# Kernel optimization log

Measured on AMD Instinct MI355X. Metric: run time of the kernel, lower is better.

Reference implementation:

```python
import jax, jax.numpy as jnp
import numpy as np

NEG_INF = -1e9  # matches masked_fill value in torch code
LRELU_ALPHA = 0.2


def setup_inputs() -> dict:
    key = jax.random.key(0)
    k1, k2, k3, k4 = jax.random.split(key, 4)
    B, N, F_IN, H, DK = 4, 2048, 128, 4, 32
    x = jax.random.normal(k1, (B, N, F_IN), dtype=jnp.float32)
    adj = jax.random.randint(k2, (B, N, N), 0, 2, dtype=jnp.int32)
    # xavier-ish scaled params
    W = jax.random.normal(k3, (H, F_IN, DK), dtype=jnp.float32) * (1.0 / np.sqrt(F_IN))
    a = jax.random.normal(k4, (H, 2 * DK, 1), dtype=jnp.float32) * (1.0 / np.sqrt(2 * DK))
    return {"x": x, "adj": adj, "W": W, "a": a}


def reference(x, adj, W, a):
    B, N, _ = x.shape
    H, _, DK = W.shape
    # h: (B, H, N, DK)
    h = jnp.einsum('bni,hio->bhno', x, W)
    # Split attention vector: e[b,h,i,j] = h_i.a_l + h_j.a_r  (avoids O(N^2 * 2d) concat)
    a_l = a[:, :DK, 0]   # (H, DK)
    a_r = a[:, DK:, 0]   # (H, DK)
    el = jnp.einsum('bhnd,hd->bhn', h, a_l)  # (B, H, N)
    er = jnp.einsum('bhnd,hd->bhn', h, a_r)  # (B, H, N)
    e = el[:, :, :, None] + er[:, :, None, :]          # (B, H, N, N)
    e = jax.nn.leaky_relu(e, negative_slope=LRELU_ALPHA)
    e = jnp.where(adj[:, None, :, :] == 0, NEG_INF, e)
    alpha = jax.nn.softmax(e, axis=-1)                 # dropout is identity (eval)
    h_prime = jnp.einsum('bhij,bhjd->bhid', alpha, h)  # (B, H, N, DK)
    # torch code does h_prime.view(B, N, -1) on contiguous (B,H,N,DK): raw reshape
    out = h_prime.reshape(B, N, H * DK)
    return out
```

## Files before the change

kernel.cpp:

```cpp
#include <hip/hip_runtime.h>
#include <stdint.h>

#define LOG2E 1.4426950408889634f

typedef __bf16 v8bf __attribute__((ext_vector_type(8)));
typedef float v16f __attribute__((ext_vector_type(16)));

static constexpr int B = 4, N = 2048, FIN = 128, H = 4, DK = 32;
static constexpr int IT = N / 32;

__device__ __forceinline__ float exp2_fast(float x) {
#if __has_builtin(__builtin_amdgcn_exp2f)
  return __builtin_amdgcn_exp2f(x);
#else
  float r;
  asm("v_exp_f32 %0, %1" : "=v"(r) : "v"(x));
  return r;
#endif
}

__device__ __forceinline__ unsigned int bf16_rne(float f) {
  unsigned int u = __builtin_bit_cast(unsigned int, f);
  u += 0x7FFFu + ((u >> 16) & 1u);
  return u >> 16;
}

__global__ __launch_bounds__(256) void k_prep(const float* __restrict__ x,
                                              const float* __restrict__ W,
                                              unsigned short* __restrict__ xb,
                                              unsigned short* __restrict__ wtb) {
  int idx = blockIdx.x * 256 + threadIdx.x;
  constexpr int TX = B * N * FIN;
  if (idx < TX) {
    xb[idx] = (unsigned short)bf16_rne(x[idx]);
  } else {
    int j = idx - TX;
    int h = j >> 12, r = j & 4095, d = r >> 7, f = r & 127;
    wtb[j] = (unsigned short)bf16_rne(W[(h * FIN + f) * DK + d]);
  }
}

__global__ __launch_bounds__(256) void k_pack(const int* __restrict__ adj,
                                              unsigned int* __restrict__ adjb) {
  int wid = (blockIdx.x * 256 + threadIdx.x) >> 6;
  int lane = threadIdx.x & 63;
  const int* p = adj + (size_t)wid * 256 + lane;
  unsigned long long m0 = __ballot(p[0] != 0);
  unsigned long long m1 = __ballot(p[64] != 0);
  unsigned long long m2 = __ballot(p[128] != 0);
  unsigned long long m3 = __ballot(p[192] != 0);
  if (lane == 0) {
    uint4 v0 = {(unsigned)m0, (unsigned)(m0 >> 32), (unsigned)m1, (unsigned)(m1 >> 32)};
    uint4 v1 = {(unsigned)m2, (unsigned)(m2 >> 32), (unsigned)m3, (unsigned)(m3 >> 32)};
    uint4* dst = (uint4*)(adjb + (size_t)wid * 8);
    dst[0] = v0;
    dst[1] = v1;
  }
}

__global__ __launch_bounds__(256) void k_hproj(const unsigned short* __restrict__ xb,
                                               const unsigned short* __restrict__ wtb,
                                               const float* __restrict__ a,
                                               unsigned short* __restrict__ h_t,
                                               float* __restrict__ el,
                                               float* __restrict__ er) {
  int blk = blockIdx.x;
  int b = blk >> 6, it = blk & 63;
  int tid = threadIdx.x;
  int head = tid >> 6, lane = tid & 63;
  int lrow = lane & 31, kh = lane >> 5;
  int bh = b * H + head;
  int n = it * 32 + lrow;
  const unsigned short* xp = xb + (b * N + n) * FIN + kh * 8;
  const unsigned short* wp = wtb + (head * DK + lrow) * FIN + kh * 8;
  v16f acc = {};
#pragma unroll
  for (int s = 0; s < FIN / 16; ++s) {
    v8bf av = __builtin_bit_cast(v8bf, *(const int4*)(wp + s * 16));
    v8bf bv = __builtin_bit_cast(v8bf, *(const int4*)(xp + s * 16));
    acc = __builtin_amdgcn_mfma_f32_32x32x16_bf16(av, bv, acc, 0, 0, 0);
  }
  float pel = 0.f, per = 0.f;
#pragma unroll
  for (int r = 0; r < 16; ++r) {
    int d = (r & 3) + 8 * (r >> 2) + 4 * kh;
    float hv = acc[r];
    h_t[(bh * DK + d) * N + n] = (unsigned short)bf16_rne(hv);
    pel = fmaf(hv, a[head * 2 * DK + d], pel);
    per = fmaf(hv, a[head * 2 * DK + DK + d], per);
  }
  pel += __shfl_xor(pel, 32);
  per += __shfl_xor(per, 32);
  if (kh == 0) {
    el[bh * N + n] = pel * LOG2E;
    er[bh * N + n] = per * LOG2E;
  }
}

__global__ __launch_bounds__(1024, 4) void k_attn(const unsigned int* __restrict__ adjb,
                                                  const unsigned short* __restrict__ h_t,
                                                  const float* __restrict__ el,
                                                  const float* __restrict__ er,
                                                  float* __restrict__ out) {
  __shared__ float part[H][1024];
  __shared__ float lsh[H][32];
  int blk = blockIdx.x;
  int b = blk >> 6, it = blk & 63;
  int tid = threadIdx.x;
  int wave = tid >> 6;
  int head = wave & 3, jq = wave >> 2;
  int lane = tid & 63, lrow = lane & 31, kh = lane >> 5;
  int ig = it * 32 + lrow, bh = b * H + head;

  part[tid >> 8][tid & 255] = 0.f;
  part[tid >> 8][256 + (tid & 255)] = 0.f;
  part[tid >> 8][512 + (tid & 255)] = 0.f;
  part[tid >> 8][768 + (tid & 255)] = 0.f;
  if (tid < H * 32) lsh[tid >> 5][tid & 31] = 0.f;

  float eli = el[bh * N + ig];
  int j0 = jq * 512 + kh * 8;
  const float* erp = er + bh * N + j0;
  const unsigned short* hp = h_t + (size_t)(bh * DK + lrow) * N + j0;

  const uint4* abp = (const uint4*)(adjb + (size_t)(b * N + ig) * 64 + jq * 16);
  uint4 ab0 = abp[0], ab1 = abp[1], ab2 = abp[2], ab3 = abp[3];
  unsigned adw[16] = {ab0.x, ab0.y, ab0.z, ab0.w, ab1.x, ab1.y, ab1.z, ab1.w,
                      ab2.x, ab2.y, ab2.z, ab2.w, ab3.x, ab3.y, ab3.z, ab3.w};
  int shkh = kh * 8;

  __syncthreads();

  v16f acc = {};
  float lsum = 0.f;
  float4 Ea = *(const float4*)erp;
  float4 Eb = *(const float4*)(erp + 4);
  int4 Hb = *(const int4*)hp;
#pragma unroll
  for (int s = 0; s < 32; ++s) {
    float4 ea = Ea, eb = Eb;
    int4 hb = Hb;
    if (s + 1 < 32) {
      int o = (s + 1) * 16;
      Ea = *(const float4*)(erp + o);
      Eb = *(const float4*)(erp + o + 4);
      Hb = *(const int4*)(hp + o);
    }
    unsigned mb = (adw[s >> 1] >> (((s & 1) * 16) + shkh)) & 0xFFu;
    float ev[8] = {ea.x, ea.y, ea.z, ea.w, eb.x, eb.y, eb.z, eb.w};
    unsigned ub[8];
#pragma unroll
    for (int k = 0; k < 8; ++k) {
      float tt = eli + ev[k];
      tt = fmaxf(tt, 0.2f * tt);
      float pv = exp2_fast(tt);
      unsigned u = __builtin_bit_cast(unsigned, pv) & 0xFFFF0000u;
      u = (mb & (1u << k)) ? u : 0u;
      ub[k] = u;
      lsum += __builtin_bit_cast(float, u);
    }
    unsigned u0 = __builtin_amdgcn_perm(ub[1], ub[0], 0x07060302u);
    unsigned u1 = __builtin_amdgcn_perm(ub[3], ub[2], 0x07060302u);
    unsigned u2 = __builtin_amdgcn_perm(ub[5], ub[4], 0x07060302u);
    unsigned u3 = __builtin_amdgcn_perm(ub[7], ub[6], 0x07060302u);
    uint4 au = {u0, u1, u2, u3};
    v8bf av = __builtin_bit_cast(v8bf, au);
    v8bf hv = __builtin_bit_cast(v8bf, hb);
    acc = __builtin_amdgcn_mfma_f32_32x32x16_bf16(av, hv, acc, 0, 0, 0);
  }

  lsum += __shfl_xor(lsum, 32);
  if (lane < 32) atomicAdd(&lsh[head][lane], lsum);
#pragma unroll
  for (int r = 0; r < 16; ++r) {
    int rowl = (r & 3) + 8 * (r >> 2) + 4 * kh;
    atomicAdd(&part[head][rowl * 32 + lrow], acc[r]);
  }
  __syncthreads();

  int e = tid * 4;
  int rh = e >> 10;
  int ri = (e >> 5) & 31;
  int rd = e & 31;
  float4 s4 = *(const float4*)&part[rh][ri * 32 + rd];
  float inv = 1.0f / lsh[rh][ri];
  float4 o;
  o.x = s4.x * inv;
  o.y = s4.y * inv;
  o.z = s4.z * inv;
  o.w = s4.w * inv;
  *(float4*)&out[(size_t)((b * H + rh) * N + it * 32 + ri) * DK + rd] = o;
}

extern "C" void kernel_launch(void* const* d_in, const int* in_sizes, int n_in,
                              void* d_out, int out_size, void* d_ws, size_t ws_size,
                              hipStream_t stream) {
  const float* x = (const float*)d_in[0];
  const int* adj = (const int*)d_in[1];
  const float* W = (const float*)d_in[2];
  const float* a = (const float*)d_in[3];
  float* out = (float*)d_out;
  char* ws = (char*)d_ws;

  unsigned short* h_t = (unsigned short*)(ws);
  float* el = (float*)(ws + 0x200000);
  float* er = (float*)(ws + 0x220000);
  unsigned short* wtb = (unsigned short*)(ws + 0x240000);
  unsigned int* adjb = (unsigned int*)(ws + 0x250000);
  unsigned short* xb = (unsigned short*)(ws + 0x450000);

  hipLaunchKernelGGL(k_pack, dim3(B * N * N / 256 / 4), dim3(256), 0, stream, adj, adjb);
  hipLaunchKernelGGL(k_prep, dim3((B * N * FIN + H * DK * FIN) / 256), dim3(256), 0, stream,
                     x, W, xb, wtb);
  hipLaunchKernelGGL(k_hproj, dim3(B * IT), dim3(256), 0, stream, xb, wtb, a, h_t, el, er);
  hipLaunchKernelGGL(k_attn, dim3(B * IT), dim3(1024), 0, stream, adjb, h_t, el, er, out);
}
```

Measured before the change: 144.4 us.

## Read int32 adjacency directly in attention kernel and split key range across two blocks

Removes the separate adjacency bit-packing kernel, so the attention kernel reads the int32 adjacency matrix directly with prefetched vector loads. This avoids a full extra pass over the 64MB adjacency plus the packed write and readback. It also doubles the grid by splitting the key dimension in half per block, swaps shared-memory atomics for per-wave partial buffers summed at the end, and adds a small final kernel that combines the two halves and normalises. The cost is that each attention wave now pulls 16x more adjacency bytes inside the hot loop, plus an extra launch and partial-sum traffic.

```diff
diff --git a/kernel.cpp b/kernel.cpp
--- a/kernel.cpp
+++ b/kernel.cpp
@@ -37,24 +37,6 @@
     int j = idx - TX;
     int h = j >> 12, r = j & 4095, d = r >> 7, f = r & 127;
     wtb[j] = (unsigned short)bf16_rne(W[(h * FIN + f) * DK + d]);
-  }
-}
-
-__global__ __launch_bounds__(256) void k_pack(const int* __restrict__ adj,
-                                              unsigned int* __restrict__ adjb) {
-  int wid = (blockIdx.x * 256 + threadIdx.x) >> 6;
-  int lane = threadIdx.x & 63;
-  const int* p = adj + (size_t)wid * 256 + lane;
-  unsigned long long m0 = __ballot(p[0] != 0);
-  unsigned long long m1 = __ballot(p[64] != 0);
-  unsigned long long m2 = __ballot(p[128] != 0);
-  unsigned long long m3 = __ballot(p[192] != 0);
-  if (lane == 0) {
-    uint4 v0 = {(unsigned)m0, (unsigned)(m0 >> 32), (unsigned)m1, (unsigned)(m1 >> 32)};
-    uint4 v1 = {(unsigned)m2, (unsigned)(m2 >> 32), (unsigned)m3, (unsigned)(m3 >> 32)};
-    uint4* dst = (uint4*)(adjb + (size_t)wid * 8);
-    dst[0] = v0;
-    dst[1] = v1;
   }
 }
 
@@ -97,57 +79,46 @@
   }
 }
 
-__global__ __launch_bounds__(1024, 4) void k_attn(const unsigned int* __restrict__ adjb,
+__global__ __launch_bounds__(1024, 8) void k_attn(const int* __restrict__ adj,
                                                   const unsigned short* __restrict__ h_t,
                                                   const float* __restrict__ el,
                                                   const float* __restrict__ er,
-                                                  float* __restrict__ out) {
-  __shared__ float part[H][1024];
-  __shared__ float lsh[H][32];
+                                                  float* __restrict__ pnum,
+                                                  float* __restrict__ pden) {
+  __shared__ float part4[4][H][1024];
+  __shared__ float lsh4[4][H][32];
   int blk = blockIdx.x;
-  int b = blk >> 6, it = blk & 63;
+  int bit = blk >> 1, jh = blk & 1;
+  int b = bit >> 6, it = bit & 63;
   int tid = threadIdx.x;
   int wave = tid >> 6;
   int head = wave & 3, jq = wave >> 2;
   int lane = tid & 63, lrow = lane & 31, kh = lane >> 5;
   int ig = it * 32 + lrow, bh = b * H + head;
 
-  part[tid >> 8][tid & 255] = 0.f;
-  part[tid >> 8][256 + (tid & 255)] = 0.f;
-  part[tid >> 8][512 + (tid & 255)] = 0.f;
-  part[tid >> 8][768 + (tid & 255)] = 0.f;
-  if (tid < H * 32) lsh[tid >> 5][tid & 31] = 0.f;
-
   float eli = el[bh * N + ig];
-  int j0 = jq * 512 + kh * 8;
+  int j0 = jh * 1024 + jq * 256 + kh * 8;
   const float* erp = er + bh * N + j0;
   const unsigned short* hp = h_t + (size_t)(bh * DK + lrow) * N + j0;
-
-  const uint4* abp = (const uint4*)(adjb + (size_t)(b * N + ig) * 64 + jq * 16);
-  uint4 ab0 = abp[0], ab1 = abp[1], ab2 = abp[2], ab3 = abp[3];
-  unsigned adw[16] = {ab0.x, ab0.y, ab0.z, ab0.w, ab1.x, ab1.y, ab1.z, ab1.w,
-                      ab2.x, ab2.y, ab2.z, ab2.w, ab3.x, ab3.y, ab3.z, ab3.w};
-  int shkh = kh * 8;
-
-  __syncthreads();
+  const int* ap = adj + ((size_t)(b * N + ig)) * N + j0;
 
   v16f acc = {};
   float lsum = 0.f;
-  float4 Ea = *(const float4*)erp;
-  float4 Eb = *(const float4*)(erp + 4);
-  int4 Hb = *(const int4*)hp;
-#pragma unroll
-  for (int s = 0; s < 32; ++s) {
-    float4 ea = Ea, eb = Eb;
-    int4 hb = Hb;
-    if (s + 1 < 32) {
-      int o = (s + 1) * 16;
-      Ea = *(const float4*)(erp + o);
-      Eb = *(const float4*)(erp + o + 4);
-      Hb = *(const int4*)(hp + o);
+  int4 A0 = *(const int4*)ap;
+  int4 A1 = *(const int4*)(ap + 4);
+#pragma unroll
+  for (int s = 0; s < 16; ++s) {
+    int o = s * 16;
+    int4 a0 = A0, a1 = A1;
+    if (s + 1 < 16) {
+      A0 = *(const int4*)(ap + o + 16);
+      A1 = *(const int4*)(ap + o + 20);
     }
-    unsigned mb = (adw[s >> 1] >> (((s & 1) * 16) + shkh)) & 0xFFu;
+    float4 ea = *(const float4*)(erp + o);
+    float4 eb = *(const float4*)(erp + o + 4);
+    int4 hb = *(const int4*)(hp + o);
     float ev[8] = {ea.x, ea.y, ea.z, ea.w, eb.x, eb.y, eb.z, eb.w};
+    int aw[8] = {a0.x, a0.y, a0.z, a0.w, a1.x, a1.y, a1.z, a1.w};
     unsigned ub[8];
 #pragma unroll
     for (int k = 0; k < 8; ++k) {
@@ -155,7 +126,7 @@
       tt = fmaxf(tt, 0.2f * tt);
       float pv = exp2_fast(tt);
       unsigned u = __builtin_bit_cast(unsigned, pv) & 0xFFFF0000u;
-      u = (mb & (1u << k)) ? u : 0u;
+      u = aw[k] ? u : 0u;
       ub[k] = u;
       lsum += __builtin_bit_cast(float, u);
     }
@@ -170,25 +141,51 @@
   }
 
   lsum += __shfl_xor(lsum, 32);
-  if (lane < 32) atomicAdd(&lsh[head][lane], lsum);
+  if (lane < 32) lsh4[jq][head][lane] = lsum;
 #pragma unroll
   for (int r = 0; r < 16; ++r) {
     int rowl = (r & 3) + 8 * (r >> 2) + 4 * kh;
-    atomicAdd(&part[head][rowl * 32 + lrow], acc[r]);
+    part4[jq][head][rowl * 32 + lrow] = acc[r];
   }
   __syncthreads();
 
   int e = tid * 4;
-  int rh = e >> 10;
-  int ri = (e >> 5) & 31;
-  int rd = e & 31;
-  float4 s4 = *(const float4*)&part[rh][ri * 32 + rd];
-  float inv = 1.0f / lsh[rh][ri];
+  int rh = e >> 10, rr = e & 1023;
+  float4 q0 = *(const float4*)&part4[0][rh][rr];
+  float4 q1 = *(const float4*)&part4[1][rh][rr];
+  float4 q2 = *(const float4*)&part4[2][rh][rr];
+  float4 q3 = *(const float4*)&part4[3][rh][rr];
+  float4 s4;
+  s4.x = (q0.x + q1.x) + (q2.x + q3.x);
+  s4.y = (q0.y + q1.y) + (q2.y + q3.y);
+  s4.z = (q0.z + q1.z) + (q2.z + q3.z);
+  s4.w = (q0.w + q1.w) + (q2.w + q3.w);
+  *(float4*)&pnum[(size_t)blk * 4096 + e] = s4;
+  if (tid < 128) {
+    float d = (lsh4[0][tid >> 5][tid & 31] + lsh4[1][tid >> 5][tid & 31]) +
+              (lsh4[2][tid >> 5][tid & 31] + lsh4[3][tid >> 5][tid & 31]);
+    pden[blk * 128 + tid] = d;
+  }
+}
+
+__global__ __launch_bounds__(1024) void k_final(const float* __restrict__ pnum,
+                                                const float* __restrict__ pden,
+                                                float* __restrict__ out) {
+  int bit = blockIdx.x;
+  int b = bit >> 6, it = bit & 63;
+  int tid = threadIdx.x;
+  int e = tid * 4;
+  int rh = e >> 10, ri = (e >> 5) & 31, rd = e & 31;
+  size_t p0 = (size_t)(bit * 2) * 4096 + e;
+  float4 n0 = *(const float4*)&pnum[p0];
+  float4 n1 = *(const float4*)&pnum[p0 + 4096];
+  float d = pden[bit * 2 * 128 + rh * 32 + ri] + pden[(bit * 2 + 1) * 128 + rh * 32 + ri];
+  float inv = 1.0f / d;
   float4 o;
-  o.x = s4.x * inv;
-  o.y = s4.y * inv;
-  o.z = s4.z * inv;
-  o.w = s4.w * inv;
+  o.x = (n0.x + n1.x) * inv;
+  o.y = (n0.y + n1.y) * inv;
+  o.z = (n0.z + n1.z) * inv;
+  o.w = (n0.w + n1.w) * inv;
   *(float4*)&out[(size_t)((b * H + rh) * N + it * 32 + ri) * DK + rd] = o;
 }
 
@@ -206,12 +203,13 @@
   float* el = (float*)(ws + 0x200000);
   float* er = (float*)(ws + 0x220000);
   unsigned short* wtb = (unsigned short*)(ws + 0x240000);
-  unsigned int* adjb = (unsigned int*)(ws + 0x250000);
-  unsigned short* xb = (unsigned short*)(ws + 0x450000);
-
-  hipLaunchKernelGGL(k_pack, dim3(B * N * N / 256 / 4), dim3(256), 0, stream, adj, adjb);
+  unsigned short* xb = (unsigned short*)(ws + 0x250000);
+  float* pnum = (float*)(ws + 0x450000);
+  float* pden = (float*)(ws + 0xC50000);
+
   hipLaunchKernelGGL(k_prep, dim3((B * N * FIN + H * DK * FIN) / 256), dim3(256), 0, stream,
                      x, W, xb, wtb);
   hipLaunchKernelGGL(k_hproj, dim3(B * IT), dim3(256), 0, stream, xb, wtb, a, h_t, el, er);
-  hipLaunchKernelGGL(k_attn, dim3(B * IT), dim3(1024), 0, stream, adjb, h_t, el, er, out);
-}
+  hipLaunchKernelGGL(k_attn, dim3(B * IT * 2), dim3(1024), 0, stream, adj, h_t, el, er, pnum, pden);
+  hipLaunchKernelGGL(k_final, dim3(B * IT), dim3(1024), 0, stream, pnum, pden, out);
+}
```

Result: slower. 158.2 us (+9.6%).
